# Performance work log

Hardware: AMD Instinct MI355X
Metric: run time of the kernel (lower is better)

The kernel has to match this reference:

```python
import jax, jax.numpy as jnp
import numpy as np

NUM_EXPERTS = 8
TOP_K = 2
HIDDEN = 768
FFN = 3072
B, S = 4, 4096


def setup_inputs() -> dict:
    key = jax.random.key(0)
    ks = jax.random.split(key, 7)
    scale_h = 1.0 / np.sqrt(HIDDEN)
    scale_f = 1.0 / np.sqrt(FFN)
    return {
        "hidden_states": jax.random.normal(ks[0], (B, S, HIDDEN), dtype=jnp.float32),
        "router_w": jax.random.normal(ks[1], (HIDDEN, NUM_EXPERTS), dtype=jnp.float32) * scale_h,
        "router_b": jnp.zeros((NUM_EXPERTS,), dtype=jnp.float32),
        "w1": jax.random.normal(ks[2], (NUM_EXPERTS, HIDDEN, FFN), dtype=jnp.float32) * scale_h,
        "b1": jnp.zeros((NUM_EXPERTS, FFN), dtype=jnp.float32),
        "w2": jax.random.normal(ks[3], (NUM_EXPERTS, FFN, HIDDEN), dtype=jnp.float32) * scale_f,
        "b2": jnp.zeros((NUM_EXPERTS, HIDDEN), dtype=jnp.float32),
    }


def _moe_forward(x_flat, router_w, router_b, w1, b1, w2, b2):
    T = x_flat.shape[0]
    # Router: logits [T, E]
    router_logits = x_flat @ router_w + router_b
    routing_weights = jax.nn.softmax(router_logits, axis=-1)
    # Top-k gating: softmax over the selected top-k logits
    top_vals, top_idx = jax.lax.top_k(router_logits, TOP_K)
    top_gates = jax.nn.softmax(top_vals, axis=-1)
    # Scatter gates into dense dispatch mask [T, E]
    rows = jnp.arange(T)[:, None]
    dispatch_mask = jnp.zeros_like(routing_weights).at[rows, top_idx].set(top_gates)
    # Expert computation: combined = sum_e gate[:, e] * FFN_e(x)
    # (tokens with zero gate contribute exactly 0, matching the torch scatter-combine)
    combined = jnp.zeros_like(x_flat)
    for e in range(NUM_EXPERTS):
        h = jax.nn.gelu(x_flat @ w1[e] + b1[e])  # [T, FFN]
        y = h @ w2[e] + b2[e]                    # [T, HIDDEN]
        combined = combined + dispatch_mask[:, e:e + 1] * y
    # Auxiliary load-balancing loss
    mean_routing_prob = jnp.mean(routing_weights, axis=0)
    tokens_per_expert = jnp.sum(dispatch_mask, axis=0) / T
    aux_loss = jnp.sum(mean_routing_prob * tokens_per_expert) * NUM_EXPERTS
    return combined, routing_weights, dispatch_mask, aux_loss, router_logits


def reference(hidden_states, router_w, router_b, w1, b1, w2, b2):
    batch, seq, hid = hidden_states.shape
    x_flat = hidden_states.reshape(-1, hid)
    combined, routing_weights, dispatch_mask, aux_loss, router_logits = _moe_forward(
        x_flat, router_w, router_b, w1, b1, w2, b2)
    E = NUM_EXPERTS
    return (
        combined.reshape(batch, seq, hid),            # expert_outputs
        routing_weights.reshape(batch, seq, E),       # routing_weights
        dispatch_mask.reshape(batch, seq, E),         # dispatch_mask
        aux_loss,                                     # aux_loss
        router_logits.reshape(batch, seq, E),         # router_logits
    )
```

## Files before the change

### kernel.cpp

```cpp
#include <hip/hip_runtime.h>
#include <math.h>

#define TOKENS 16384
#define HID 768
#define FFN_DIM 3072
#define NEXP 8
#define MAXT 136

#define RT_TPB 128
#define RT_BLOCKS (TOKENS / RT_TPB)

typedef __bf16 bf16x8 __attribute__((ext_vector_type(8)));
typedef float f32x4 __attribute__((ext_vector_type(4)));

#define GLOBAL_AS(p) ((const __attribute__((address_space(1))) void*)(p))
#define LDS_AS(p)    ((__attribute__((address_space(3))) void*)(p))
#define SB0 __builtin_amdgcn_sched_barrier(0)

__device__ __forceinline__ float gelu_f(float x) {
    const float x3 = x * x * x;
    const float z = 0.7978845608028654f * (x + 0.044715f * x3);
    const float e = __expf(2.f * z);
    const float t = 1.f - 2.f / (e + 1.f);
    return 0.5f * x * (1.f + t);
}

__device__ __forceinline__ unsigned short f2bf(float v) {
    return __builtin_bit_cast(unsigned short, (__bf16)v);
}

__global__ void __launch_bounds__(512) router_kernel(
    const float* __restrict__ x, const float* __restrict__ rw,
    const float* __restrict__ rb,
    float* __restrict__ out_rw, float* __restrict__ out_dm,
    float* __restrict__ out_logits,
    int* __restrict__ counts, float* __restrict__ probsum,
    float* __restrict__ gatesum, int* __restrict__ lists,
    float* __restrict__ glists)
{
    __shared__ int s_cnt[NEXP], s_base[NEXP];
    __shared__ float s_prob[NEXP], s_gate[NEXP];
    __shared__ int s_e1[RT_TPB], s_s1[RT_TPB], s_e2[RT_TPB], s_s2[RT_TPB];
    __shared__ float s_g1v[RT_TPB], s_g2v[RT_TPB];

    const int tid = threadIdx.x;
    if (tid < NEXP) { s_cnt[tid] = 0; s_prob[tid] = 0.f; s_gate[tid] = 0.f; }
    __syncthreads();

    const int wave = tid >> 6, lane = tid & 63;

    for (int it = 0; it < RT_TPB / 8; ++it) {
        const int lt = wave * (RT_TPB / 8) + it;
        const int t = blockIdx.x * RT_TPB + lt;
        const float* xr = x + (size_t)t * HID;
        float acc[NEXP];
#pragma unroll
        for (int e = 0; e < NEXP; ++e) acc[e] = 0.f;
#pragma unroll
        for (int j = 0; j < 12; ++j) {
            const int i = lane + (j << 6);
            const float xv = xr[i];
            const float4 a = ((const float4*)(rw + (size_t)i * NEXP))[0];
            const float4 b = ((const float4*)(rw + (size_t)i * NEXP))[1];
            acc[0] += xv * a.x; acc[1] += xv * a.y; acc[2] += xv * a.z; acc[3] += xv * a.w;
            acc[4] += xv * b.x; acc[5] += xv * b.y; acc[6] += xv * b.z; acc[7] += xv * b.w;
        }
#pragma unroll
        for (int off = 32; off > 0; off >>= 1)
#pragma unroll
            for (int e = 0; e < NEXP; ++e) acc[e] += __shfl_down(acc[e], off, 64);

        if (lane == 0) {
            float lg[NEXP];
            float m = -1e30f;
#pragma unroll
            for (int e = 0; e < NEXP; ++e) { lg[e] = acc[e] + rb[e]; m = fmaxf(m, lg[e]); }
            float ex[NEXP]; float s = 0.f;
#pragma unroll
            for (int e = 0; e < NEXP; ++e) { ex[e] = expf(lg[e] - m); s += ex[e]; }
            const float inv = 1.f / s;
            float* lrow = out_logits + (size_t)t * NEXP;
            float* prow = out_rw + (size_t)t * NEXP;
#pragma unroll
            for (int e = 0; e < NEXP; ++e) {
                lrow[e] = lg[e];
                const float p = ex[e] * inv;
                prow[e] = p;
                atomicAdd(&s_prob[e], p);
            }
            int i1 = 0;
#pragma unroll
            for (int e = 1; e < NEXP; ++e) if (lg[e] > lg[i1]) i1 = e;
            int i2 = (i1 == 0) ? 1 : 0;
#pragma unroll
            for (int e = 0; e < NEXP; ++e) if (e != i1 && lg[e] > lg[i2]) i2 = e;
            const float e2 = expf(lg[i2] - lg[i1]);
            const float g1 = 1.f / (1.f + e2);
            const float g2 = e2 / (1.f + e2);
            out_dm[(size_t)t * NEXP + i1] = g1;
            out_dm[(size_t)t * NEXP + i2] = g2;
            atomicAdd(&s_gate[i1], g1);
            atomicAdd(&s_gate[i2], g2);
            s_e1[lt] = i1; s_s1[lt] = atomicAdd(&s_cnt[i1], 1); s_g1v[lt] = g1;
            s_e2[lt] = i2; s_s2[lt] = atomicAdd(&s_cnt[i2], 1); s_g2v[lt] = g2;
        }
    }
    __syncthreads();
    if (tid < NEXP) {
        s_base[tid] = atomicAdd(&counts[tid], s_cnt[tid]);
        atomicAdd(&probsum[tid], s_prob[tid]);
        atomicAdd(&gatesum[tid], s_gate[tid]);
    }
    __syncthreads();
    if (tid < RT_TPB) {
        const int t = blockIdx.x * RT_TPB + tid;
        int e = s_e1[tid]; int p = s_base[e] + s_s1[tid];
        lists[e * TOKENS + p] = t; glists[e * TOKENS + p] = s_g1v[tid];
        e = s_e2[tid]; p = s_base[e] + s_s2[tid];
        lists[e * TOKENS + p] = t; glists[e * TOKENS + p] = s_g2v[tid];
    }
}

__global__ void finalize_kernel(const int* __restrict__ counts,
                                const float* __restrict__ probsum,
                                const float* __restrict__ gatesum,
                                int* __restrict__ poffs,
                                float* __restrict__ out_aux)
{
    if (threadIdx.x == 0 && blockIdx.x == 0) {
        float s = 0.f; int po = 0;
        for (int e = 0; e < NEXP; ++e) {
            poffs[e] = po;
            po += ((counts[e] + 255) >> 8) << 8;
            s += (probsum[e] / (float)TOKENS) * (gatesum[e] / (float)TOKENS);
        }
        poffs[NEXP] = po;
        *out_aux = s * (float)NEXP;
    }
}

__global__ void __launch_bounds__(192) gatherx_kernel(
    const float* __restrict__ x, const int* __restrict__ counts,
    const int* __restrict__ poffs, const int* __restrict__ lists,
    unsigned short* __restrict__ Xg)
{
    const int r = blockIdx.x;
    if (r >= poffs[NEXP]) return;
    int e = 0;
#pragma unroll
    for (int q = 1; q < NEXP; ++q) e += (r >= poffs[q]);
    const int ri = r - poffs[e];
    const int tid = threadIdx.x;
    uint2 o = make_uint2(0u, 0u);
    if (ri < counts[e]) {
        const int tok = lists[e * TOKENS + ri];
        const float4 v = *(const float4*)&x[(size_t)tok * HID + tid * 4];
        o.x = (unsigned)f2bf(v.x) | ((unsigned)f2bf(v.y) << 16);
        o.y = (unsigned)f2bf(v.z) | ((unsigned)f2bf(v.w) << 16);
    }
    *(uint2*)&Xg[(size_t)r * HID + tid * 4] = o;
}

__global__ void __launch_bounds__(256) convT_kernel(const float* __restrict__ in,
                                                    unsigned short* __restrict__ out,
                                                    int R, int C)
{
    __shared__ float sT[32][65];
    const int e = blockIdx.z;
    const float* in_e = in + (size_t)e * R * C;
    unsigned short* out_e = out + (size_t)e * R * C;
    const int r0 = blockIdx.y * 64;
    const int c0 = blockIdx.x * 32;
    const int tid = threadIdx.x;
    const int rr = tid >> 3, c4 = (tid & 7) * 4;
#pragma unroll
    for (int half = 0; half < 2; ++half) {
        const int r = rr + half * 32;
        const float4 v = *(const float4*)&in_e[(size_t)(r0 + r) * C + c0 + c4];
        sT[c4 + 0][r] = v.x; sT[c4 + 1][r] = v.y;
        sT[c4 + 2][r] = v.z; sT[c4 + 3][r] = v.w;
    }
    __syncthreads();
    const int c = tid >> 3, u = tid & 7;
    uint4 pk;
    const float* sr = &sT[c][u * 8];
    pk.x = (unsigned)f2bf(sr[0]) | ((unsigned)f2bf(sr[1]) << 16);
    pk.y = (unsigned)f2bf(sr[2]) | ((unsigned)f2bf(sr[3]) << 16);
    pk.z = (unsigned)f2bf(sr[4]) | ((unsigned)f2bf(sr[5]) << 16);
    pk.w = (unsigned)f2bf(sr[6]) | ((unsigned)f2bf(sr[7]) << 16);
    *(uint4*)&out_e[(size_t)(c0 + c) * R + r0 + u * 8] = pk;
}


#define STAGE_AB(os_, kt_) do {                                                                          \
    const unsigned short* _a = aSrc + (kt_) * 64;                                                        \
    const unsigned short* _b = bSrc + (kt_) * 64;                                                        \
    __builtin_amdgcn_global_load_lds(GLOBAL_AS(_a + (size_t)(wv*32 +  0) * KS), LDS_AS(&lds[(os_) +         (wv*32 +  0) * 64]), 16, 0, 0); \
    __builtin_amdgcn_global_load_lds(GLOBAL_AS(_a + (size_t)(wv*32 +  8) * KS), LDS_AS(&lds[(os_) +         (wv*32 +  8) * 64]), 16, 0, 0); \
    __builtin_amdgcn_global_load_lds(GLOBAL_AS(_a + (size_t)(wv*32 + 16) * KS), LDS_AS(&lds[(os_) +         (wv*32 + 16) * 64]), 16, 0, 0); \
    __builtin_amdgcn_global_load_lds(GLOBAL_AS(_a + (size_t)(wv*32 + 24) * KS), LDS_AS(&lds[(os_) +         (wv*32 + 24) * 64]), 16, 0, 0); \
    __builtin_amdgcn_global_load_lds(GLOBAL_AS(_b + (size_t)(wv*16 +  0) * KS), LDS_AS(&lds[(os_) + 16384 + (wv*16 +  0) * 64]), 16, 0, 0); \
    __builtin_amdgcn_global_load_lds(GLOBAL_AS(_b + (size_t)(wv*16 +  8) * KS), LDS_AS(&lds[(os_) + 16384 + (wv*16 +  8) * 64]), 16, 0, 0); \
} while (0)

#define DECODE_TILE(NT_) \
    const int nwg = gridDim.x;                                                       \
    const int orig = blockIdx.x;                                                     \
    const int qq = nwg >> 3, rr2 = nwg & 7;                                          \
    const int xcd = orig & 7, pos = orig >> 3;                                       \
    const int wid = (xcd < rr2 ? xcd * (qq + 1) : rr2 * (qq + 1) + (xcd - rr2) * qq) + pos; \
    const int nSuper = tilesPG >> 3;                                                 \
    const int fullB = nSuper * 8 * (NT_);                                            \
    int mt, nti;                                                                     \
    if (wid < fullB) {                                                               \
        const int st = wid / (8 * (NT_));                                            \
        const int lo = wid - st * (8 * (NT_));                                       \
        mt = (st << 3) + (lo & 7);                                                   \
        nti = lo >> 3;                                                               \
    } else {                                                                         \
        const int rem = tilesPG - (nSuper << 3);                                     \
        const int lo = wid - fullB;                                                  \
        mt = (nSuper << 3) + lo % rem;                                               \
        nti = lo / rem;                                                              \
    }

__global__ void __launch_bounds__(512, 2) gemm1_kernel(
    const unsigned short* __restrict__ Xg, const unsigned short* __restrict__ W1T,
    const float* __restrict__ b1, const int* __restrict__ poffs,
    unsigned short* __restrict__ H, int grBase, int tilesPG)
{
    extern __shared__ __bf16 lds[];
    const int KS = HID;
    const int NK = HID / 64;

    DECODE_TILE(FFN_DIM / 128)
    const int gr = grBase + mt * 256;
    if (gr >= poffs[NEXP]) return;
    int e = 0;
#pragma unroll
    for (int q = 1; q < NEXP; ++q) e += (gr >= poffs[q]);
    const int hbase = gr - grBase;
    const int n0 = nti * 128;

    const int tid = threadIdx.x;
    const int wv = tid >> 6, lane = tid & 63;
    const int wr = wv >> 2, wc = wv & 3;
    const int fr = lane & 15, q4 = lane >> 4, sw = fr & 7;
    const int rlo = lane >> 3;
    const int cswz = ((lane & 7) ^ rlo) << 3;

    const unsigned short* aSrc = Xg + (size_t)(gr + rlo) * KS + cswz;
    const unsigned short* bSrc = W1T + (size_t)e * (HID * FFN_DIM) + (size_t)(n0 + rlo) * KS + cswz;

    const int aRow = (wr * 128 + fr) * 64;
    const int bRow = (wc * 32 + fr) * 64;
    const int c0 = (q4 ^ sw) << 3;
    const int c1 = ((4 + q4) ^ sw) << 3;

    f32x4 acc[8][2];
#pragma unroll
    for (int i = 0; i < 8; ++i) { acc[i][0] = (f32x4)(0.f); acc[i][1] = (f32x4)(0.f); }

    int oc = 0, on = 24576, os = 49152;
    STAGE_AB(oc, 0);
    STAGE_AB(on, 1);
    asm volatile("s_waitcnt vmcnt(6)" ::: "memory");
    SB0; __builtin_amdgcn_s_barrier(); SB0;

    for (int kt = 0; kt < NK; ++kt) {
        if (kt + 2 < NK) STAGE_AB(os, kt + 2);
        __builtin_amdgcn_s_setprio(1);
        const bf16x8 b00 = *(const bf16x8*)&lds[oc + 16384 + bRow + c0];
        const bf16x8 b01 = *(const bf16x8*)&lds[oc + 16384 + bRow + c1];
        const bf16x8 b10 = *(const bf16x8*)&lds[oc + 16384 + bRow + 1024 + c0];
        const bf16x8 b11 = *(const bf16x8*)&lds[oc + 16384 + bRow + 1024 + c1];
#pragma unroll
        for (int mi = 0; mi < 8; ++mi) {
            const bf16x8 a0 = *(const bf16x8*)&lds[oc + aRow + mi * 1024 + c0];
            const bf16x8 a1 = *(const bf16x8*)&lds[oc + aRow + mi * 1024 + c1];
            acc[mi][0] = __builtin_amdgcn_mfma_f32_16x16x32_bf16(a0, b00, acc[mi][0], 0, 0, 0);
            acc[mi][0] = __builtin_amdgcn_mfma_f32_16x16x32_bf16(a1, b01, acc[mi][0], 0, 0, 0);
            acc[mi][1] = __builtin_amdgcn_mfma_f32_16x16x32_bf16(a0, b10, acc[mi][1], 0, 0, 0);
            acc[mi][1] = __builtin_amdgcn_mfma_f32_16x16x32_bf16(a1, b11, acc[mi][1], 0, 0, 0);
        }
        __builtin_amdgcn_s_setprio(0);
        if (kt + 1 < NK) {
            SB0;
            if (kt + 2 < NK) asm volatile("s_waitcnt vmcnt(6)" ::: "memory");
            else             asm volatile("s_waitcnt vmcnt(0)" ::: "memory");
            __builtin_amdgcn_s_barrier(); SB0;
        }
        const int t_ = oc; oc = on; on = os; os = t_;
    }

    const float* b1e = b1 + (size_t)e * FFN_DIM;
    const float bias0 = b1e[n0 + wc * 32 + fr];
    const float bias1 = b1e[n0 + wc * 32 + 16 + fr];
    unsigned short* Hcol = H + (size_t)hbase * FFN_DIM + n0 + wc * 32 + fr;
#pragma unroll
    for (int mi = 0; mi < 8; ++mi) {
#pragma unroll
        for (int r = 0; r < 4; ++r) {
            const int m = wr * 128 + mi * 16 + q4 * 4 + r;
            unsigned short* hp = Hcol + (size_t)m * FFN_DIM;
            hp[0]  = f2bf(gelu_f(acc[mi][0][r] + bias0));
            hp[16] = f2bf(gelu_f(acc[mi][1][r] + bias1));
        }
    }
}

__global__ void __launch_bounds__(512, 2) gemm2_kernel(
    const unsigned short* __restrict__ H, const unsigned short* __restrict__ W2T,
    const float* __restrict__ b2, const int* __restrict__ counts,
    const int* __restrict__ poffs, const int* __restrict__ lists,
    const float* __restrict__ glists, float* __restrict__ out,
    int grBase, int tilesPG)
{
    extern __shared__ __bf16 lds[];
    const int KS = FFN_DIM;
    const int NK = FFN_DIM / 64;

    DECODE_TILE(HID / 128)
    const int gr = grBase + mt * 256;
    if (gr >= poffs[NEXP]) return;
    int e = 0;
#pragma unroll
    for (int q = 1; q < NEXP; ++q) e += (gr >= poffs[q]);
    const int cnt = counts[e];
    const int m0 = gr - poffs[e];
    const int hbase = gr - grBase;
    const int n0 = nti * 128;

    const int tid = threadIdx.x;
    const int wv = tid >> 6, lane = tid & 63;
    const int wr = wv >> 2, wc = wv & 3;
    const int fr = lane & 15, q4 = lane >> 4, sw = fr & 7;
    const int rlo = lane >> 3;
    const int cswz = ((lane & 7) ^ rlo) << 3;

    const unsigned short* aSrc = H + (size_t)(hbase + rlo) * KS + cswz;
    const unsigned short* bSrc = W2T + (size_t)e * (HID * FFN_DIM) + (size_t)(n0 + rlo) * KS + cswz;

    const int aRow = (wr * 128 + fr) * 64;
    const int bRow = (wc * 32 + fr) * 64;
    const int c0 = (q4 ^ sw) << 3;
    const int c1 = ((4 + q4) ^ sw) << 3;

    f32x4 acc[8][2];
#pragma unroll
    for (int i = 0; i < 8; ++i) { acc[i][0] = (f32x4)(0.f); acc[i][1] = (f32x4)(0.f); }

    int oc = 0, on = 24576, os = 49152;
    STAGE_AB(oc, 0);
    STAGE_AB(on, 1);
    asm volatile("s_waitcnt vmcnt(6)" ::: "memory");
    SB0; __builtin_amdgcn_s_barrier(); SB0;

    for (int kt = 0; kt < NK; ++kt) {
        if (kt + 2 < NK) STAGE_AB(os, kt + 2);
        __builtin_amdgcn_s_setprio(1);
        const bf16x8 b00 = *(const bf16x8*)&lds[oc + 16384 + bRow + c0];
        const bf16x8 b01 = *(const bf16x8*)&lds[oc + 16384 + bRow + c1];
        const bf16x8 b10 = *(const bf16x8*)&lds[oc + 16384 + bRow + 1024 + c0];
        const bf16x8 b11 = *(const bf16x8*)&lds[oc + 16384 + bRow + 1024 + c1];
#pragma unroll
        for (int mi = 0; mi < 8; ++mi) {
            const bf16x8 a0 = *(const bf16x8*)&lds[oc + aRow + mi * 1024 + c0];
            const bf16x8 a1 = *(const bf16x8*)&lds[oc + aRow + mi * 1024 + c1];
            acc[mi][0] = __builtin_amdgcn_mfma_f32_16x16x32_bf16(a0, b00, acc[mi][0], 0, 0, 0);
            acc[mi][0] = __builtin_amdgcn_mfma_f32_16x16x32_bf16(a1, b01, acc[mi][0], 0, 0, 0);
            acc[mi][1] = __builtin_amdgcn_mfma_f32_16x16x32_bf16(a0, b10, acc[mi][1], 0, 0, 0);
            acc[mi][1] = __builtin_amdgcn_mfma_f32_16x16x32_bf16(a1, b11, acc[mi][1], 0, 0, 0);
        }
        __builtin_amdgcn_s_setprio(0);
        if (kt + 1 < NK) {
            SB0;
            if (kt + 2 < NK) asm volatile("s_waitcnt vmcnt(6)" ::: "memory");
            else             asm volatile("s_waitcnt vmcnt(0)" ::: "memory");
            __builtin_amdgcn_s_barrier(); SB0;
        }
        const int t_ = oc; oc = on; on = os; os = t_;
    }

    int* sTok = (int*)(lds + 73728);
    float* sGate = (float*)(lds + 73728 + 512);
    if (tid < 256) {
        int ri = m0 + tid; if (ri > cnt - 1) ri = cnt - 1;
        sTok[tid] = lists[e * TOKENS + ri];
        sGate[tid] = glists[e * TOKENS + ri];
    }
    __syncthreads();

    const float* b2e = b2 + (size_t)e * HID;
    const float bias0 = b2e[n0 + wc * 32 + fr];
    const float bias1 = b2e[n0 + wc * 32 + 16 + fr];
#pragma unroll
    for (int mi = 0; mi < 8; ++mi) {
#pragma unroll
        for (int r = 0; r < 4; ++r) {
            const int m = wr * 128 + mi * 16 + q4 * 4 + r;
            if (m0 + m < cnt) {
                const int tok = sTok[m];
                const float g = sGate[m];
                float* orow = out + (size_t)tok * HID + n0 + wc * 32 + fr;
                atomicAdd(orow,      g * (acc[mi][0][r] + bias0));
                atomicAdd(orow + 16, g * (acc[mi][1][r] + bias1));
            }
        }
    }
}

#define BM 16
#define KC 64
#define XS 772
#define HS 68
__global__ void __launch_bounds__(256) ffn_kernel(
    const float* __restrict__ x, const float* __restrict__ w1,
    const float* __restrict__ b1, const float* __restrict__ w2,
    const float* __restrict__ b2, const int* __restrict__ counts,
    const int* __restrict__ lists, const float* __restrict__ glists,
    float* __restrict__ out)
{
    const int e = blockIdx.y;
    const int count = counts[e];
    const int row0 = blockIdx.x * BM;
    if (row0 >= count) return;

    __shared__ float sX[BM * XS];
    __shared__ float sH[BM * HS];
    __shared__ int sTokF[BM];
    __shared__ float sGateF[BM];
    const int tid = threadIdx.x;

    if (tid < BM) {
        const int ri = row0 + tid;
        int tok = 0; float g = 0.f;
        if (ri < count) { tok = lists[e * TOKENS + ri]; g = glists[e * TOKENS + ri]; }
        sTokF[tid] = tok; sGateF[tid] = g;
    }
    __syncthreads();
    {
        const int r = tid >> 4, q = tid & 15;
        const float4* src = (const float4*)(x + (size_t)sTokF[r] * HID);
#pragma unroll
        for (int j = 0; j < 12; ++j) {
            const float4 v = src[q + (j << 4)];
            *(float4*)&sX[r * XS + ((q + (j << 4)) << 2)] = v;
        }
    }
    __syncthreads();

    const float* w1e = w1 + (size_t)e * HID * FFN_DIM;
    const float* w2e = w2 + (size_t)e * FFN_DIM * HID;
    const float* b1e = b1 + (size_t)e * FFN_DIM;
    const float* b2e = b2 + (size_t)e * HID;
    const int r1 = tid & 15;
    const int c0 = (tid >> 4) << 2;
    const int c2 = (tid >> 4) * 48;

    float Y[48];
#pragma unroll
    for (int j = 0; j < 48; ++j) Y[j] = 0.f;

    for (int ch = 0; ch < FFN_DIM / KC; ++ch) {
        float h0 = 0.f, h1 = 0.f, h2 = 0.f, h3 = 0.f;
        const float* w1c = w1e + ch * KC + c0;
        for (int i = 0; i < HID; i += 4) {
            const float4 xv = *(const float4*)&sX[r1 * XS + i];
            const float* wp = w1c + (size_t)i * FFN_DIM;
            const float4 wa = *(const float4*)(wp);
            const float4 wb = *(const float4*)(wp + FFN_DIM);
            const float4 wc = *(const float4*)(wp + 2 * FFN_DIM);
            const float4 wd = *(const float4*)(wp + 3 * FFN_DIM);
            h0 += xv.x * wa.x + xv.y * wb.x + xv.z * wc.x + xv.w * wd.x;
            h1 += xv.x * wa.y + xv.y * wb.y + xv.z * wc.y + xv.w * wd.y;
            h2 += xv.x * wa.z + xv.y * wb.z + xv.z * wc.z + xv.w * wd.z;
            h3 += xv.x * wa.w + xv.y * wb.w + xv.z * wc.w + xv.w * wd.w;
        }
        const int cb = ch * KC + c0;
        h0 = gelu_f(h0 + b1e[cb + 0]);
        h1 = gelu_f(h1 + b1e[cb + 1]);
        h2 = gelu_f(h2 + b1e[cb + 2]);
        h3 = gelu_f(h3 + b1e[cb + 3]);
        __syncthreads();
        *(float4*)&sH[r1 * HS + c0] = make_float4(h0, h1, h2, h3);
        __syncthreads();
        const float* w2c = w2e + (size_t)ch * KC * HID + c2;
        for (int k = 0; k < KC; ++k) {
            const float hv = sH[r1 * HS + k];
            const float4* wr = (const float4*)(w2c + (size_t)k * HID);
#pragma unroll
            for (int j4 = 0; j4 < 12; ++j4) {
                const float4 wv = wr[j4];
                Y[j4 * 4 + 0] += hv * wv.x;
                Y[j4 * 4 + 1] += hv * wv.y;
                Y[j4 * 4 + 2] += hv * wv.z;
                Y[j4 * 4 + 3] += hv * wv.w;
            }
        }
    }
    const int ri = row0 + r1;
    if (ri < count) {
        const float g = sGateF[r1];
        float* orow = out + (size_t)sTokF[r1] * HID + c2;
#pragma unroll
        for (int j = 0; j < 48; ++j)
            atomicAdd(&orow[j], g * (Y[j] + b2e[c2 + j]));
    }
}

extern "C" void kernel_launch(void* const* d_in, const int* in_sizes, int n_in,
                              void* d_out, int out_size, void* d_ws, size_t ws_size,
                              hipStream_t stream)
{
    const float* x  = (const float*)d_in[0];
    const float* rw = (const float*)d_in[1];
    const float* rb = (const float*)d_in[2];
    const float* w1 = (const float*)d_in[3];
    const float* b1 = (const float*)d_in[4];
    const float* w2 = (const float*)d_in[5];
    const float* b2 = (const float*)d_in[6];

    float* out = (float*)d_out;
    float* out_comb   = out;
    float* out_rw     = out + (size_t)TOKENS * HID;
    float* out_dm     = out_rw + (size_t)TOKENS * NEXP;
    float* out_aux    = out_dm + (size_t)TOKENS * NEXP;
    float* out_logits = out_aux + 1;

    char* ws = (char*)d_ws;
    int*   counts  = (int*)ws;
    int*   poffs   = (int*)(ws + 64);
    float* probsum = (float*)(ws + 128);
    float* gatesum = (float*)(ws + 160);
    int*   lists   = (int*)(ws + 256);
    float* glists  = (float*)(ws + 256 + (size_t)NEXP * TOKENS * 4);
    size_t off = 256 + (size_t)NEXP * TOKENS * 8;
    off = (off + 255) & ~(size_t)255;
    unsigned short* Xg  = (unsigned short*)(ws + off); off += (size_t)MAXT * 256 * HID * 2;
    unsigned short* W1T = (unsigned short*)(ws + off); off += (size_t)NEXP * HID * FFN_DIM * 2;
    unsigned short* W2T = (unsigned short*)(ws + off); off += (size_t)NEXP * HID * FFN_DIM * 2;
    unsigned short* Hbuf = (unsigned short*)(ws + off);

    size_t avail = (ws_size > off) ? (ws_size - off) : 0;
    const int tilesFit = (int)(avail / ((size_t)256 * FFN_DIM * 2));
    int G = 0, tilesPG = 0;
    if (tilesFit >= 1) {
        G = (MAXT + tilesFit - 1) / tilesFit;
        tilesPG = (MAXT + G - 1) / G;
    }

    hipMemsetAsync(out_comb, 0, (size_t)TOKENS * HID * sizeof(float), stream);
    hipMemsetAsync(out_dm, 0, (size_t)TOKENS * NEXP * sizeof(float), stream);
    hipMemsetAsync(d_ws, 0, 256, stream);

    router_kernel<<<dim3(RT_BLOCKS), 512, 0, stream>>>(
        x, rw, rb, out_rw, out_dm, out_logits,
        counts, probsum, gatesum, lists, glists);
    finalize_kernel<<<1, 64, 0, stream>>>(counts, probsum, gatesum, poffs, out_aux);

    if (G > 0) {
        static int attr_done = 0;
        if (!attr_done) {
            hipFuncSetAttribute((const void*)gemm1_kernel,
                                hipFuncAttributeMaxDynamicSharedMemorySize, 147456);
            hipFuncSetAttribute((const void*)gemm2_kernel,
                                hipFuncAttributeMaxDynamicSharedMemorySize, 149504);
            attr_done = 1;
        }
        gatherx_kernel<<<dim3(MAXT * 256), 192, 0, stream>>>(
            x, counts, poffs, lists, Xg);
        convT_kernel<<<dim3(FFN_DIM / 32, HID / 64, NEXP), 256, 0, stream>>>(w1, W1T, HID, FFN_DIM);
        convT_kernel<<<dim3(HID / 32, FFN_DIM / 64, NEXP), 256, 0, stream>>>(w2, W2T, FFN_DIM, HID);
        for (int g = 0; g < G; ++g) {
            const int grBase = g * tilesPG * 256;
            gemm1_kernel<<<dim3(tilesPG * (FFN_DIM / 128)), 512, 147456, stream>>>(
                Xg, W1T, b1, poffs, Hbuf, grBase, tilesPG);
            gemm2_kernel<<<dim3(tilesPG * (HID / 128)), 512, 149504, stream>>>(
                Hbuf, W2T, b2, counts, poffs, lists, glists, out_comb, grBase, tilesPG);
        }
    } else {
        ffn_kernel<<<dim3(TOKENS / BM, NEXP), 256, 0, stream>>>(
            x, w1, b1, w2, b2, counts, lists, glists, out_comb);
    }
}
```

Measured before the change: 836.4 us.

## Widen GEMM tiles to 256x256 with phased double-buffered half-K staging

Both expert GEMMs move from 256x128 to 256x256 output tiles, giving each wave a 128x64 sub-tile with 32 accumulators. The K-loop becomes double-buffered with 32-wide K halves, split into four phases that interleave staging loads with MFMA work under barriers. The aim is more operand reuse per LDS read and fewer global loads per FLOP, at the cost of more accumulator registers, half as many workgroups and extra barriers. The LDS budget changes accordingly.

```diff
diff --git a/kernel.cpp b/kernel.cpp
--- a/kernel.cpp
+++ b/kernel.cpp
@@ -16,6 +16,8 @@
 #define GLOBAL_AS(p) ((const __attribute__((address_space(1))) void*)(p))
 #define LDS_AS(p)    ((__attribute__((address_space(3))) void*)(p))
 #define SB0 __builtin_amdgcn_sched_barrier(0)
+#define VM4 asm volatile("s_waitcnt vmcnt(4)" ::: "memory")
+#define VM0 asm volatile("s_waitcnt vmcnt(0)" ::: "memory")
 
 __device__ __forceinline__ float gelu_f(float x) {
     const float x3 = x * x * x;
@@ -192,15 +194,42 @@
 }
 
 
-#define STAGE_AB(os_, kt_) do {                                                                          \
-    const unsigned short* _a = aSrc + (kt_) * 64;                                                        \
-    const unsigned short* _b = bSrc + (kt_) * 64;                                                        \
-    __builtin_amdgcn_global_load_lds(GLOBAL_AS(_a + (size_t)(wv*32 +  0) * KS), LDS_AS(&lds[(os_) +         (wv*32 +  0) * 64]), 16, 0, 0); \
-    __builtin_amdgcn_global_load_lds(GLOBAL_AS(_a + (size_t)(wv*32 +  8) * KS), LDS_AS(&lds[(os_) +         (wv*32 +  8) * 64]), 16, 0, 0); \
-    __builtin_amdgcn_global_load_lds(GLOBAL_AS(_a + (size_t)(wv*32 + 16) * KS), LDS_AS(&lds[(os_) +         (wv*32 + 16) * 64]), 16, 0, 0); \
-    __builtin_amdgcn_global_load_lds(GLOBAL_AS(_a + (size_t)(wv*32 + 24) * KS), LDS_AS(&lds[(os_) +         (wv*32 + 24) * 64]), 16, 0, 0); \
-    __builtin_amdgcn_global_load_lds(GLOBAL_AS(_b + (size_t)(wv*16 +  0) * KS), LDS_AS(&lds[(os_) + 16384 + (wv*16 +  0) * 64]), 16, 0, 0); \
-    __builtin_amdgcn_global_load_lds(GLOBAL_AS(_b + (size_t)(wv*16 +  8) * KS), LDS_AS(&lds[(os_) + 16384 + (wv*16 +  8) * 64]), 16, 0, 0); \
+#define STAGE_A(bufE_, kt_, kh_) do { \
+    const unsigned short* _p = aStP + (size_t)(kt_) * 64 + (kh_) * 32; \
+    __bf16* _d = &lds[(bufE_) + (kh_) * 8192 + wv * 1024]; \
+    __builtin_amdgcn_global_load_lds(GLOBAL_AS(_p), LDS_AS(_d), 16, 0, 0); \
+    __builtin_amdgcn_global_load_lds(GLOBAL_AS(_p + 16 * KS), LDS_AS(_d + 512), 16, 0, 0); \
+} while (0)
+
+#define STAGE_B(bufE_, kt_, kh_) do { \
+    const unsigned short* _p = bStP + (size_t)(kt_) * 64 + (kh_) * 32; \
+    __bf16* _d = &lds[(bufE_) + 16384 + (kh_) * 8192 + wv * 1024]; \
+    __builtin_amdgcn_global_load_lds(GLOBAL_AS(_p), LDS_AS(_d), 16, 0, 0); \
+    __builtin_amdgcn_global_load_lds(GLOBAL_AS(_p + 16 * KS), LDS_AS(_d + 512), 16, 0, 0); \
+} while (0)
+
+#define PH(MH, KH, READB, STG, VMS) do { \
+    bf16x8 a_[4]; \
+    _Pragma("unroll") \
+    for (int _j = 0; _j < 4; ++_j) \
+        a_[_j] = *(const bf16x8*)&lds[cE + (KH) * 8192 + aRd + ((MH) * 4 + _j) * 512]; \
+    if (READB) { \
+        _Pragma("unroll") \
+        for (int _n = 0; _n < 4; ++_n) \
+            b_[_n] = *(const bf16x8*)&lds[cE + (KH) * 8192 + bRd + _n * 512]; \
+    } \
+    STG; \
+    VMS; \
+    SB0; __builtin_amdgcn_s_barrier(); SB0; \
+    __builtin_amdgcn_s_setprio(1); \
+    _Pragma("unroll") \
+    for (int _j = 0; _j < 4; ++_j) \
+        _Pragma("unroll") \
+        for (int _n = 0; _n < 4; ++_n) \
+            acc[(MH) * 4 + _j][_n] = __builtin_amdgcn_mfma_f32_16x16x32_bf16( \
+                a_[_j], b_[_n], acc[(MH) * 4 + _j][_n], 0, 0, 0); \
+    __builtin_amdgcn_s_setprio(0); \
+    SB0; __builtin_amdgcn_s_barrier(); SB0; \
 } while (0)
 
 #define DECODE_TILE(NT_) \
@@ -213,9 +242,9 @@
     const int fullB = nSuper * 8 * (NT_);                                            \
     int mt, nti;                                                                     \
     if (wid < fullB) {                                                               \
-        const int st = wid / (8 * (NT_));                                            \
-        const int lo = wid - st * (8 * (NT_));                                       \
-        mt = (st << 3) + (lo & 7);                                                   \
+        const int st_ = wid / (8 * (NT_));                                           \
+        const int lo = wid - st_ * (8 * (NT_));                                      \
+        mt = (st_ << 3) + (lo & 7);                                                  \
         nti = lo >> 3;                                                               \
     } else {                                                                         \
         const int rem = tilesPG - (nSuper << 3);                                     \
@@ -231,80 +260,68 @@
 {
     extern __shared__ __bf16 lds[];
     const int KS = HID;
-    const int NK = HID / 64;
-
-    DECODE_TILE(FFN_DIM / 128)
+    const int NKT = HID / 64;
+
+    DECODE_TILE(FFN_DIM / 256)
     const int gr = grBase + mt * 256;
     if (gr >= poffs[NEXP]) return;
     int e = 0;
 #pragma unroll
     for (int q = 1; q < NEXP; ++q) e += (gr >= poffs[q]);
     const int hbase = gr - grBase;
-    const int n0 = nti * 128;
+    const int n0 = nti * 256;
 
     const int tid = threadIdx.x;
     const int wv = tid >> 6, lane = tid & 63;
     const int wr = wv >> 2, wc = wv & 3;
-    const int fr = lane & 15, q4 = lane >> 4, sw = fr & 7;
-    const int rlo = lane >> 3;
-    const int cswz = ((lane & 7) ^ rlo) << 3;
-
-    const unsigned short* aSrc = Xg + (size_t)(gr + rlo) * KS + cswz;
-    const unsigned short* bSrc = W1T + (size_t)e * (HID * FFN_DIM) + (size_t)(n0 + rlo) * KS + cswz;
-
-    const int aRow = (wr * 128 + fr) * 64;
-    const int bRow = (wc * 32 + fr) * 64;
-    const int c0 = (q4 ^ sw) << 3;
-    const int c1 = ((4 + q4) ^ sw) << 3;
-
-    f32x4 acc[8][2];
-#pragma unroll
-    for (int i = 0; i < 8; ++i) { acc[i][0] = (f32x4)(0.f); acc[i][1] = (f32x4)(0.f); }
-
-    int oc = 0, on = 24576, os = 49152;
-    STAGE_AB(oc, 0);
-    STAGE_AB(on, 1);
-    asm volatile("s_waitcnt vmcnt(6)" ::: "memory");
+    const int fr = lane & 15, q4 = lane >> 4;
+    const int rowoff = lane >> 2;
+    const int swzW = ((lane & 3) ^ ((lane >> 3) & 3)) << 3;
+    const int swzR = ((q4 ^ ((fr >> 1) & 3)) << 3);
+
+    const unsigned short* aStP = Xg + (size_t)(gr + wv * 32 + rowoff) * KS + swzW;
+    const unsigned short* bStP = W1T + (size_t)e * (HID * FFN_DIM)
+                               + (size_t)(n0 + wv * 32 + rowoff) * KS + swzW;
+
+    const int aRd = (wr * 128 + fr) * 32 + swzR;
+    const int bRd = 16384 + (wc * 64 + fr) * 32 + swzR;
+
+    f32x4 acc[8][4];
+#pragma unroll
+    for (int i = 0; i < 8; ++i)
+#pragma unroll
+        for (int j = 0; j < 4; ++j) acc[i][j] = (f32x4)(0.f);
+    bf16x8 b_[4];
+
+    STAGE_A(0, 0, 0); STAGE_B(0, 0, 0); STAGE_A(0, 0, 1); STAGE_B(0, 0, 1);
+    VM4;
     SB0; __builtin_amdgcn_s_barrier(); SB0;
 
-    for (int kt = 0; kt < NK; ++kt) {
-        if (kt + 2 < NK) STAGE_AB(os, kt + 2);
-        __builtin_amdgcn_s_setprio(1);
-        const bf16x8 b00 = *(const bf16x8*)&lds[oc + 16384 + bRow + c0];
-        const bf16x8 b01 = *(const bf16x8*)&lds[oc + 16384 + bRow + c1];
-        const bf16x8 b10 = *(const bf16x8*)&lds[oc + 16384 + bRow + 1024 + c0];
-        const bf16x8 b11 = *(const bf16x8*)&lds[oc + 16384 + bRow + 1024 + c1];
-#pragma unroll
-        for (int mi = 0; mi < 8; ++mi) {
-            const bf16x8 a0 = *(const bf16x8*)&lds[oc + aRow + mi * 1024 + c0];
-            const bf16x8 a1 = *(const bf16x8*)&lds[oc + aRow + mi * 1024 + c1];
-            acc[mi][0] = __builtin_amdgcn_mfma_f32_16x16x32_bf16(a0, b00, acc[mi][0], 0, 0, 0);
-            acc[mi][0] = __builtin_amdgcn_mfma_f32_16x16x32_bf16(a1, b01, acc[mi][0], 0, 0, 0);
-            acc[mi][1] = __builtin_amdgcn_mfma_f32_16x16x32_bf16(a0, b10, acc[mi][1], 0, 0, 0);
-            acc[mi][1] = __builtin_amdgcn_mfma_f32_16x16x32_bf16(a1, b11, acc[mi][1], 0, 0, 0);
-        }
-        __builtin_amdgcn_s_setprio(0);
-        if (kt + 1 < NK) {
-            SB0;
-            if (kt + 2 < NK) asm volatile("s_waitcnt vmcnt(6)" ::: "memory");
-            else             asm volatile("s_waitcnt vmcnt(0)" ::: "memory");
-            __builtin_amdgcn_s_barrier(); SB0;
-        }
-        const int t_ = oc; oc = on; on = os; os = t_;
+#pragma unroll 2
+    for (int kt = 0; kt < NKT; ++kt) {
+        const int cE = (kt & 1) << 15;
+        const int nE = cE ^ 32768;
+        const int kn = kt + 1;
+        const bool st = (kn < NKT);
+        PH(0, 0, 1, if (st) STAGE_A(nE, kn, 0), ((void)0));
+        PH(1, 0, 0, if (st) STAGE_B(nE, kn, 0), if (st) { VM4; } else { VM0; });
+        PH(0, 1, 1, if (st) STAGE_A(nE, kn, 1), ((void)0));
+        PH(1, 1, 0, if (st) STAGE_B(nE, kn, 1), if (st) { VM4; });
     }
 
     const float* b1e = b1 + (size_t)e * FFN_DIM;
-    const float bias0 = b1e[n0 + wc * 32 + fr];
-    const float bias1 = b1e[n0 + wc * 32 + 16 + fr];
-    unsigned short* Hcol = H + (size_t)hbase * FFN_DIM + n0 + wc * 32 + fr;
+    float bias[4];
+#pragma unroll
+    for (int nj = 0; nj < 4; ++nj) bias[nj] = b1e[n0 + wc * 64 + nj * 16 + fr];
 #pragma unroll
     for (int mi = 0; mi < 8; ++mi) {
 #pragma unroll
         for (int r = 0; r < 4; ++r) {
             const int m = wr * 128 + mi * 16 + q4 * 4 + r;
-            unsigned short* hp = Hcol + (size_t)m * FFN_DIM;
-            hp[0]  = f2bf(gelu_f(acc[mi][0][r] + bias0));
-            hp[16] = f2bf(gelu_f(acc[mi][1][r] + bias1));
+            unsigned short* hp = H + (size_t)(hbase + m) * FFN_DIM + n0 + wc * 64 + fr;
+#pragma unroll
+            for (int nj = 0; nj < 4; ++nj)
+                hp[nj * 16] = f2bf(gelu_f(acc[mi][nj][r] + bias[nj]));
         }
     }
 }
@@ -318,9 +335,9 @@
 {
     extern __shared__ __bf16 lds[];
     const int KS = FFN_DIM;
-    const int NK = FFN_DIM / 64;
-
-    DECODE_TILE(HID / 128)
+    const int NKT = FFN_DIM / 64;
+
+    DECODE_TILE(HID / 256)
     const int gr = grBase + mt * 256;
     if (gr >= poffs[NEXP]) return;
     int e = 0;
@@ -329,61 +346,48 @@
     const int cnt = counts[e];
     const int m0 = gr - poffs[e];
     const int hbase = gr - grBase;
-    const int n0 = nti * 128;
+    const int n0 = nti * 256;
 
     const int tid = threadIdx.x;
     const int wv = tid >> 6, lane = tid & 63;
     const int wr = wv >> 2, wc = wv & 3;
-    const int fr = lane & 15, q4 = lane >> 4, sw = fr & 7;
-    const int rlo = lane >> 3;
-    const int cswz = ((lane & 7) ^ rlo) << 3;
-
-    const unsigned short* aSrc = H + (size_t)(hbase + rlo) * KS + cswz;
-    const unsigned short* bSrc = W2T + (size_t)e * (HID * FFN_DIM) + (size_t)(n0 + rlo) * KS + cswz;
-
-    const int aRow = (wr * 128 + fr) * 64;
-    const int bRow = (wc * 32 + fr) * 64;
-    const int c0 = (q4 ^ sw) << 3;
-    const int c1 = ((4 + q4) ^ sw) << 3;
-
-    f32x4 acc[8][2];
-#pragma unroll
-    for (int i = 0; i < 8; ++i) { acc[i][0] = (f32x4)(0.f); acc[i][1] = (f32x4)(0.f); }
-
-    int oc = 0, on = 24576, os = 49152;
-    STAGE_AB(oc, 0);
-    STAGE_AB(on, 1);
-    asm volatile("s_waitcnt vmcnt(6)" ::: "memory");
+    const int fr = lane & 15, q4 = lane >> 4;
+    const int rowoff = lane >> 2;
+    const int swzW = ((lane & 3) ^ ((lane >> 3) & 3)) << 3;
+    const int swzR = ((q4 ^ ((fr >> 1) & 3)) << 3);
+
+    const unsigned short* aStP = H + (size_t)(hbase + wv * 32 + rowoff) * KS + swzW;
+    const unsigned short* bStP = W2T + (size_t)e * (HID * FFN_DIM)
+                               + (size_t)(n0 + wv * 32 + rowoff) * KS + swzW;
+
+    const int aRd = (wr * 128 + fr) * 32 + swzR;
+    const int bRd = 16384 + (wc * 64 + fr) * 32 + swzR;
+
+    f32x4 acc[8][4];
+#pragma unroll
+    for (int i = 0; i < 8; ++i)
+#pragma unroll
+        for (int j = 0; j < 4; ++j) acc[i][j] = (f32x4)(0.f);
+    bf16x8 b_[4];
+
+    STAGE_A(0, 0, 0); STAGE_B(0, 0, 0); STAGE_A(0, 0, 1); STAGE_B(0, 0, 1);
+    VM4;
     SB0; __builtin_amdgcn_s_barrier(); SB0;
 
-    for (int kt = 0; kt < NK; ++kt) {
-        if (kt + 2 < NK) STAGE_AB(os, kt + 2);
-        __builtin_amdgcn_s_setprio(1);
-        const bf16x8 b00 = *(const bf16x8*)&lds[oc + 16384 + bRow + c0];
-        const bf16x8 b01 = *(const bf16x8*)&lds[oc + 16384 + bRow + c1];
-        const bf16x8 b10 = *(const bf16x8*)&lds[oc + 16384 + bRow + 1024 + c0];
-        const bf16x8 b11 = *(const bf16x8*)&lds[oc + 16384 + bRow + 1024 + c1];
-#pragma unroll
-        for (int mi = 0; mi < 8; ++mi) {
-            const bf16x8 a0 = *(const bf16x8*)&lds[oc + aRow + mi * 1024 + c0];
-            const bf16x8 a1 = *(const bf16x8*)&lds[oc + aRow + mi * 1024 + c1];
-            acc[mi][0] = __builtin_amdgcn_mfma_f32_16x16x32_bf16(a0, b00, acc[mi][0], 0, 0, 0);
-            acc[mi][0] = __builtin_amdgcn_mfma_f32_16x16x32_bf16(a1, b01, acc[mi][0], 0, 0, 0);
-            acc[mi][1] = __builtin_amdgcn_mfma_f32_16x16x32_bf16(a0, b10, acc[mi][1], 0, 0, 0);
-            acc[mi][1] = __builtin_amdgcn_mfma_f32_16x16x32_bf16(a1, b11, acc[mi][1], 0, 0, 0);
-        }
-        __builtin_amdgcn_s_setprio(0);
-        if (kt + 1 < NK) {
-            SB0;
-            if (kt + 2 < NK) asm volatile("s_waitcnt vmcnt(6)" ::: "memory");
-            else             asm volatile("s_waitcnt vmcnt(0)" ::: "memory");
-            __builtin_amdgcn_s_barrier(); SB0;
-        }
-        const int t_ = oc; oc = on; on = os; os = t_;
-    }
-
-    int* sTok = (int*)(lds + 73728);
-    float* sGate = (float*)(lds + 73728 + 512);
+#pragma unroll 2
+    for (int kt = 0; kt < NKT; ++kt) {
+        const int cE = (kt & 1) << 15;
+        const int nE = cE ^ 32768;
+        const int kn = kt + 1;
+        const bool st = (kn < NKT);
+        PH(0, 0, 1, if (st) STAGE_A(nE, kn, 0), ((void)0));
+        PH(1, 0, 0, if (st) STAGE_B(nE, kn, 0), if (st) { VM4; } else { VM0; });
+        PH(0, 1, 1, if (st) STAGE_A(nE, kn, 1), ((void)0));
+        PH(1, 1, 0, if (st) STAGE_B(nE, kn, 1), if (st) { VM4; });
+    }
+
+    int* sTok = (int*)&lds[65536];
+    float* sGate = (float*)&lds[66048];
     if (tid < 256) {
         int ri = m0 + tid; if (ri > cnt - 1) ri = cnt - 1;
         sTok[tid] = lists[e * TOKENS + ri];
@@ -392,8 +396,9 @@
     __syncthreads();
 
     const float* b2e = b2 + (size_t)e * HID;
-    const float bias0 = b2e[n0 + wc * 32 + fr];
-    const float bias1 = b2e[n0 + wc * 32 + 16 + fr];
+    float bias[4];
+#pragma unroll
+    for (int nj = 0; nj < 4; ++nj) bias[nj] = b2e[n0 + wc * 64 + nj * 16 + fr];
 #pragma unroll
     for (int mi = 0; mi < 8; ++mi) {
 #pragma unroll
@@ -402,9 +407,10 @@
             if (m0 + m < cnt) {
                 const int tok = sTok[m];
                 const float g = sGate[m];
-                float* orow = out + (size_t)tok * HID + n0 + wc * 32 + fr;
-                atomicAdd(orow,      g * (acc[mi][0][r] + bias0));
-                atomicAdd(orow + 16, g * (acc[mi][1][r] + bias1));
+                float* orow = out + (size_t)tok * HID + n0 + wc * 64 + fr;
+#pragma unroll
+                for (int nj = 0; nj < 4; ++nj)
+                    atomicAdd(&orow[nj * 16], g * (acc[mi][nj][r] + bias[nj]));
             }
         }
     }
@@ -563,9 +569,9 @@
         static int attr_done = 0;
         if (!attr_done) {
             hipFuncSetAttribute((const void*)gemm1_kernel,
-                                hipFuncAttributeMaxDynamicSharedMemorySize, 147456);
+                                hipFuncAttributeMaxDynamicSharedMemorySize, 131072);
             hipFuncSetAttribute((const void*)gemm2_kernel,
-                                hipFuncAttributeMaxDynamicSharedMemorySize, 149504);
+                                hipFuncAttributeMaxDynamicSharedMemorySize, 133120);
             attr_done = 1;
         }
         gatherx_kernel<<<dim3(MAXT * 256), 192, 0, stream>>>(
@@ -574,9 +580,9 @@
         convT_kernel<<<dim3(HID / 32, FFN_DIM / 64, NEXP), 256, 0, stream>>>(w2, W2T, FFN_DIM, HID);
         for (int g = 0; g < G; ++g) {
             const int grBase = g * tilesPG * 256;
-            gemm1_kernel<<<dim3(tilesPG * (FFN_DIM / 128)), 512, 147456, stream>>>(
+            gemm1_kernel<<<dim3(tilesPG * (FFN_DIM / 256)), 512, 131072, stream>>>(
                 Xg, W1T, b1, poffs, Hbuf, grBase, tilesPG);
-            gemm2_kernel<<<dim3(tilesPG * (HID / 128)), 512, 149504, stream>>>(
+            gemm2_kernel<<<dim3(tilesPG * (HID / 256)), 512, 133120, stream>>>(
                 Hbuf, W2T, b2, counts, poffs, lists, glists, out_comb, grBase, tilesPG);
         }
     } else {
```

Result: faster. 810.9 us (-3.1%).
